# Kernel tuning notes

Measured on AMD Instinct MI355X. Metric: run time of the kernel, lower is better.

The kernel has to match this reference:

```python
import jax, jax.numpy as jnp
import numpy as np

B, N, D, P, H = 16, 1024, 512, 512, 8
E = P // H  # head dim = 64


def layer_norm(x, g, b, eps=1e-5):
    mu = jnp.mean(x, axis=-1, keepdims=True)
    var = jnp.var(x, axis=-1, keepdims=True)
    return (x - mu) * jax.lax.rsqrt(var + eps) * g + b


def setup_inputs() -> dict:
    key = jax.random.key(0)
    ks = jax.random.split(key, 12)
    s = 0.02
    inp = {
        "x": jax.random.normal(ks[0], (B, N, D), dtype=jnp.float32),
        "Wq": jax.random.normal(ks[1], (D, P), dtype=jnp.float32) * s,
        "bq": jnp.zeros((P,), jnp.float32),
        "Wk": jax.random.normal(ks[2], (D, P), dtype=jnp.float32) * s,
        "bk": jnp.zeros((P,), jnp.float32),
        "Wv": jax.random.normal(ks[3], (D, P), dtype=jnp.float32) * s,
        "bv": jnp.zeros((P,), jnp.float32),
        "Wo": jax.random.normal(ks[4], (P, D), dtype=jnp.float32) * s,
        "bo": jnp.zeros((D,), jnp.float32),
        "ln1_g": jnp.ones((D,), jnp.float32),
        "ln1_b": jnp.zeros((D,), jnp.float32),
        "W1": jax.random.normal(ks[5], (D, 4 * D), dtype=jnp.float32) * s,
        "b1": jnp.zeros((4 * D,), jnp.float32),
        "W2": jax.random.normal(ks[6], (4 * D, D), dtype=jnp.float32) * s,
        "b2": jnp.zeros((D,), jnp.float32),
        "ln2_g": jnp.ones((D,), jnp.float32),
        "ln2_b": jnp.zeros((D,), jnp.float32),
    }
    return inp


def reference(x, Wq, bq, Wk, bk, Wv, bv, Wo, bo, ln1_g, ln1_b, W1, b1, W2, b2, ln2_g, ln2_b):
    # dropout layers are identity in eval mode
    q = (x @ Wq + bq).reshape(B, N, H, E)
    k = (x @ Wk + bk).reshape(B, N, H, E)
    v = (x @ Wv + bv).reshape(B, N, H, E)
    scale = 1.0 / jnp.sqrt(jnp.float32(E))
    scores = jnp.einsum('blhe,bshe->bhls', q, k)  # [B,H,L,S]
    A = jax.nn.softmax(scale * scores, axis=-1)
    V = jnp.einsum('bhls,bshd->blhd', A, v).reshape(B, N, P)
    att = V @ Wo + bo
    x1 = layer_norm(x + att, ln1_g, ln1_b)
    # FFN: 1x1 convs over channel dim == per-token linears, exact GELU
    ff = jax.nn.gelu(x1 @ W1 + b1, approximate=False) @ W2 + b2
    return layer_norm(x1 + ff, ln2_g, ln2_b)
```

## Files before the change

kernel.cpp:

```cpp
#include <hip/hip_runtime.h>
#include <hip/hip_bf16.h>

typedef __hip_bfloat16 bf16;
typedef __bf16 bf16x8 __attribute__((ext_vector_type(8)));
typedef __bf16 bf16x4 __attribute__((ext_vector_type(4)));
typedef float f32x4 __attribute__((ext_vector_type(4)));

static __device__ __forceinline__ f32x4 mfma16(bf16x8 a, bf16x8 b, f32x4 c) {
  return __builtin_amdgcn_mfma_f32_16x16x32_bf16(a, b, c, 0, 0, 0);
}
static __device__ __forceinline__ bf16x8 ld8(const bf16* p) {
  return *reinterpret_cast<const bf16x8*>(p);
}
static __device__ __forceinline__ float toF(float v) { return v; }
static __device__ __forceinline__ float toF(bf16 v) { return __bfloat162float(v); }
static __device__ __forceinline__ void stF(float* p, float v) { *p = v; }
static __device__ __forceinline__ void stF(bf16* p, float v) { *p = __float2bfloat16(v); }

typedef __attribute__((address_space(1))) void gvoid;
typedef __attribute__((address_space(3))) void lvoid;
static __device__ __forceinline__ void gl2lds16(const bf16* g, bf16* l) {
  __builtin_amdgcn_global_load_lds((gvoid*)g, (lvoid*)l, 16, 0, 0);
}

__global__ __launch_bounds__(256) void cvt_kernel(const float* __restrict__ in,
                                                  bf16* __restrict__ out) {
  long i = (long)blockIdx.x * 256 + threadIdx.x;
  float4 v = reinterpret_cast<const float4*>(in)[i];
  bf16x4 o;
  o[0] = __float2bfloat16(v.x); o[1] = __float2bfloat16(v.y);
  o[2] = __float2bfloat16(v.z); o[3] = __float2bfloat16(v.w);
  reinterpret_cast<bf16x4*>(out)[i] = o;
}

__global__ void prep_weights(const float* __restrict__ Wq, const float* __restrict__ Wk,
                             const float* __restrict__ Wv, const float* __restrict__ Wo,
                             const float* __restrict__ W1, const float* __restrict__ W2,
                             bf16* __restrict__ Wtqkv, bf16* __restrict__ WtO,
                             bf16* __restrict__ Wt1, bf16* __restrict__ Wt2) {
  int id = blockIdx.x;
  const float* in;
  bf16* out;
  int K, N, n0, k0;
  if (id < 1024) {
    int which = id >> 8, t = id & 255;
    K = 512; N = 512;
    n0 = (t & 15) * 32; k0 = (t >> 4) * 32;
    if (which == 0)      { in = Wq; out = Wtqkv; }
    else if (which == 1) { in = Wk; out = Wtqkv + (size_t)512 * 512; }
    else if (which == 2) { in = Wv; out = Wtqkv + (size_t)1024 * 512; }
    else                 { in = Wo; out = WtO; }
  } else if (id < 2048) {
    int t = id - 1024;
    in = W1; out = Wt1; K = 512; N = 2048;
    n0 = (t & 63) * 32; k0 = (t >> 6) * 32;
  } else {
    int t = id - 2048;
    in = W2; out = Wt2; K = 2048; N = 512;
    n0 = (t & 15) * 32; k0 = (t >> 4) * 32;
  }
  __shared__ float tile[32][33];
  int tx = threadIdx.x, ty = threadIdx.y;
#pragma unroll
  for (int j = 0; j < 32; j += 8)
    tile[ty + j][tx] = in[(long)(k0 + ty + j) * N + n0 + tx];
  __syncthreads();
#pragma unroll
  for (int j = 0; j < 32; j += 8)
    out[(long)(n0 + ty + j) * K + k0 + tx] = __float2bfloat16(tile[tx][ty + j]);
}

template <int MODE>
__global__ __launch_bounds__(256) void gemm_kernel(
    const bf16* __restrict__ A, const bf16* __restrict__ Wt,
    const float* __restrict__ b0, const float* __restrict__ b1_,
    const float* __restrict__ b2_, bf16* C0, bf16* C1, bf16* C2,
    int K, int ldc, int mmask, int mshift) {
  __shared__ alignas(16) bf16 As[2][128 * 32];
  __shared__ alignas(16) bf16 Bs[2][128 * 32];
  const int tid = threadIdx.x;
  const int wave = tid >> 6, lane = tid & 63;
  const int lr = lane & 15, lq = lane >> 4;
  const int L = blockIdx.x;
  const int m0 = (L & mmask) * 128, n0 = (L >> mshift) * 128;
  const int wm = (wave >> 1) * 64, wn = (wave & 1) * 64;

  const int srow0 = (wave * 2) * 16 + (lane >> 2);
  const int srow1 = (wave * 2 + 1) * 16 + (lane >> 2);
  const int scol = (lane & 3) * 8;
  const bf16* Ag0 = A + (long)(m0 + srow0) * K + scol;
  const bf16* Ag1 = A + (long)(m0 + srow1) * K + scol;
  const bf16* Bg0 = Wt + (long)(n0 + srow0) * K + scol;
  const bf16* Bg1 = Wt + (long)(n0 + srow1) * K + scol;
  const int so0 = (wave * 2) * 16 * 32;
  const int so1 = (wave * 2 + 1) * 16 * 32;

  f32x4 acc[4][4] = {};

  gl2lds16(Ag0, &As[0][so0]);
  gl2lds16(Ag1, &As[0][so1]);
  gl2lds16(Bg0, &Bs[0][so0]);
  gl2lds16(Bg1, &Bs[0][so1]);
  __syncthreads();

  int p = 0;
  for (int k0 = 0; k0 < K; k0 += 32) {
    int kn = k0 + 32;
    if (kn < K) {
      gl2lds16(Ag0 + kn, &As[p ^ 1][so0]);
      gl2lds16(Ag1 + kn, &As[p ^ 1][so1]);
      gl2lds16(Bg0 + kn, &Bs[p ^ 1][so0]);
      gl2lds16(Bg1 + kn, &Bs[p ^ 1][so1]);
    }
    bf16x8 af[4], bfr[4];
#pragma unroll
    for (int i = 0; i < 4; ++i) af[i] = ld8(&As[p][(wm + i * 16 + lr) * 32 + lq * 8]);
#pragma unroll
    for (int j = 0; j < 4; ++j) bfr[j] = ld8(&Bs[p][(wn + j * 16 + lr) * 32 + lq * 8]);
#pragma unroll
    for (int i = 0; i < 4; ++i)
#pragma unroll
      for (int j = 0; j < 4; ++j) acc[i][j] = mfma16(af[i], bfr[j], acc[i][j]);
    __syncthreads();
    p ^= 1;
  }

  const float* bias = b0;
  bf16* C = C0;
  int cb = n0;
  bool vmode = false;
  if (MODE == 2) {
    if (n0 >= 1024)     { bias = b2_; C = C2; cb = n0 - 1024; vmode = true; }
    else if (n0 >= 512) { bias = b1_; C = C1; cb = n0 - 512; }
  }

#pragma unroll
  for (int i = 0; i < 4; ++i) {
#pragma unroll
    for (int j = 0; j < 4; ++j) {
      int col = cb + wn + j * 16 + lr;
      float bv = bias[col];
#pragma unroll
      for (int rr = 0; rr < 4; ++rr) {
        int row = m0 + wm + i * 16 + lq * 4 + rr;
        float v = acc[i][j][rr] + bv;
        if (MODE == 1) v = 0.5f * v * (1.0f + erff(v * 0.70710678118654752f));
        if (MODE == 2 && vmode) {
          int hh = col >> 6, e = col & 63;
          int bb = row >> 10, tok = row & 1023;
          C[(((long)((bb * 8 + hh) * 64 + e)) << 10) + tok] = __float2bfloat16(v);
        } else {
          C[(long)row * ldc + col] = __float2bfloat16(v);
        }
      }
    }
  }
}

__global__ __launch_bounds__(256) void attn_splitk(
    const bf16* __restrict__ Q, const bf16* __restrict__ Km,
    const bf16* __restrict__ Vt, bf16* __restrict__ Op,
    float* __restrict__ lsum) {
  constexpr int SP = 72;
  __shared__ alignas(16) bf16 Pall[4][64 * SP];
  const int tid = threadIdx.x;
  const int wave = tid >> 6, lane = tid & 63;
  const int lr = lane & 15, lq = lane >> 4;
  const int L = blockIdx.x;
  const int bh = ((L >> 6) << 3) | (L & 7);
  const int qh = (L >> 3) & 7;
  const int qc = qh & 3, half = qh >> 2;
  const int h = bh & 7, b = bh >> 3;
  const int q0 = qc * 256 + wave * 64;
  bf16* P = Pall[wave];
  const float Cc = 0.18033688011112042f;

  bf16x8 qf[4][2];
#pragma unroll
  for (int qs = 0; qs < 4; ++qs) {
    const bf16* qrow = Q + (long)(b * 1024 + q0 + qs * 16 + lr) * 512 + h * 64;
    qf[qs][0] = ld8(qrow + lq * 8);
    qf[qs][1] = ld8(qrow + 32 + lq * 8);
  }
  const bf16* kbase = Km + (long)(b * 1024 + half * 512) * 512 + h * 64;
  const bf16* vbase = Vt + (long)((b * 8 + h) * 64) * 1024 + half * 512;

  bf16x8 ones;
#pragma unroll
  for (int k = 0; k < 8; ++k) ones[k] = __float2bfloat16(1.0f);

  f32x4 oacc[4][4] = {};
  f32x4 lacc[4] = {};

  for (int kb = 0; kb < 8; ++kb) {
#pragma unroll
    for (int kt = 0; kt < 4; ++kt) {
      const bf16* krow = kbase + (long)(kb * 64 + kt * 16 + lr) * 512;
      bf16x8 kf0 = ld8(krow + lq * 8);
      bf16x8 kf1 = ld8(krow + 32 + lq * 8);
#pragma unroll
      for (int qs = 0; qs < 4; ++qs) {
        f32x4 t = {};
        t = mfma16(kf0, qf[qs][0], t);
        t = mfma16(kf1, qf[qs][1], t);
        bf16x4 pk;
#pragma unroll
        for (int rr = 0; rr < 4; ++rr) pk[rr] = __float2bfloat16(exp2f(t[rr] * Cc));
        *reinterpret_cast<bf16x4*>(&P[(qs * 16 + lr) * SP + kt * 16 + lq * 4]) = pk;
      }
    }
    __builtin_amdgcn_sched_barrier(0);
    bf16x8 pf[4][2];
#pragma unroll
    for (int qs = 0; qs < 4; ++qs) {
      pf[qs][0] = ld8(&P[(qs * 16 + lr) * SP + lq * 8]);
      pf[qs][1] = ld8(&P[(qs * 16 + lr) * SP + 32 + lq * 8]);
    }
#pragma unroll
    for (int qs = 0; qs < 4; ++qs) {
      lacc[qs] = mfma16(pf[qs][0], ones, lacc[qs]);
      lacc[qs] = mfma16(pf[qs][1], ones, lacc[qs]);
    }
#pragma unroll
    for (int j0 = 0; j0 < 4; ++j0) {
      const bf16* vrow = vbase + (long)(j0 * 16 + lr) * 1024 + kb * 64;
      bf16x8 vf0 = ld8(vrow + lq * 8);
      bf16x8 vf1 = ld8(vrow + 32 + lq * 8);
#pragma unroll
      for (int qs = 0; qs < 4; ++qs) {
        oacc[qs][j0] = mfma16(pf[qs][0], vf0, oacc[qs][j0]);
        oacc[qs][j0] = mfma16(pf[qs][1], vf1, oacc[qs][j0]);
      }
    }
    __builtin_amdgcn_sched_barrier(0);
  }

  bf16* Oh = Op + (size_t)half * ((size_t)16384 * 512);
#pragma unroll
  for (int qs = 0; qs < 4; ++qs)
#pragma unroll
    for (int rr = 0; rr < 4; ++rr)
#pragma unroll
      for (int j0 = 0; j0 < 4; ++j0)
        Oh[(long)(b * 1024 + q0 + qs * 16 + lq * 4 + rr) * 512 + h * 64 + j0 * 16 + lr] =
            __float2bfloat16(oacc[qs][j0][rr]);
  if (lr == 0) {
    float* lp = lsum + (size_t)half * 131072 + ((size_t)(b * 8 + h) << 10);
#pragma unroll
    for (int qs = 0; qs < 4; ++qs)
#pragma unroll
      for (int rr = 0; rr < 4; ++rr)
        lp[q0 + qs * 16 + lq * 4 + rr] = lacc[qs][rr];
  }
}

__global__ __launch_bounds__(256) void attn_combine(
    const bf16* __restrict__ Op, const float* __restrict__ lsum,
    bf16* __restrict__ O) {
  long i = (long)blockIdx.x * 256 + threadIdx.x;
  long idx = i * 8;
  int tok = (int)(idx >> 9), col = (int)(idx & 511);
  int b = tok >> 10, q = tok & 1023, h = col >> 6;
  int li = (b * 8 + h) * 1024 + q;
  float inv = 1.0f / (lsum[li] + lsum[131072 + li]);
  bf16x8 a = ld8(Op + idx);
  bf16x8 c = ld8(Op + (size_t)16384 * 512 + idx);
  bf16x8 o;
#pragma unroll
  for (int k = 0; k < 8; ++k)
    o[k] = __float2bfloat16(((float)a[k] + (float)c[k]) * inv);
  *reinterpret_cast<bf16x8*>(O + idx) = o;
}

__global__ __launch_bounds__(256) void attn_kernel(
    const bf16* Q, const bf16* __restrict__ Km,
    const bf16* __restrict__ Vt, bf16* O) {
  constexpr int SP = 72;
  __shared__ alignas(16) bf16 Pall[4][64 * SP];
  const int tid = threadIdx.x;
  const int wave = tid >> 6, lane = tid & 63;
  const int lr = lane & 15, lq = lane >> 4;
  const int L = blockIdx.x;
  const int bh = ((L >> 5) << 3) | (L & 7);
  const int qc = (L >> 3) & 3;
  const int h = bh & 7, b = bh >> 3;
  const int q0 = qc * 256 + wave * 64;
  bf16* P = Pall[wave];
  const float Cc = 0.18033688011112042f;

  bf16x8 qf[4][2];
#pragma unroll
  for (int qs = 0; qs < 4; ++qs) {
    const bf16* qrow = Q + (long)(b * 1024 + q0 + qs * 16 + lr) * 512 + h * 64;
    qf[qs][0] = ld8(qrow + lq * 8);
    qf[qs][1] = ld8(qrow + 32 + lq * 8);
  }
  const bf16* kbase = Km + (long)(b * 1024) * 512 + h * 64;
  const bf16* vbase = Vt + (long)((b * 8 + h) * 64) * 1024;

  bf16x8 ones;
#pragma unroll
  for (int k = 0; k < 8; ++k) ones[k] = __float2bfloat16(1.0f);

  f32x4 oacc[4][4] = {};
  f32x4 lacc[4] = {};

  for (int kb = 0; kb < 16; ++kb) {
#pragma unroll
    for (int kt = 0; kt < 4; ++kt) {
      const bf16* krow = kbase + (long)(kb * 64 + kt * 16 + lr) * 512;
      bf16x8 kf0 = ld8(krow + lq * 8);
      bf16x8 kf1 = ld8(krow + 32 + lq * 8);
#pragma unroll
      for (int qs = 0; qs < 4; ++qs) {
        f32x4 t = {};
        t = mfma16(kf0, qf[qs][0], t);
        t = mfma16(kf1, qf[qs][1], t);
        bf16x4 pk;
#pragma unroll
        for (int rr = 0; rr < 4; ++rr) pk[rr] = __float2bfloat16(exp2f(t[rr] * Cc));
        *reinterpret_cast<bf16x4*>(&P[(qs * 16 + lr) * SP + kt * 16 + lq * 4]) = pk;
      }
    }
    __builtin_amdgcn_sched_barrier(0);
    bf16x8 pf[4][2];
#pragma unroll
    for (int qs = 0; qs < 4; ++qs) {
      pf[qs][0] = ld8(&P[(qs * 16 + lr) * SP + lq * 8]);
      pf[qs][1] = ld8(&P[(qs * 16 + lr) * SP + 32 + lq * 8]);
    }
#pragma unroll
    for (int qs = 0; qs < 4; ++qs) {
      lacc[qs] = mfma16(pf[qs][0], ones, lacc[qs]);
      lacc[qs] = mfma16(pf[qs][1], ones, lacc[qs]);
    }
#pragma unroll
    for (int j0 = 0; j0 < 4; ++j0) {
      const bf16* vrow = vbase + (long)(j0 * 16 + lr) * 1024 + kb * 64;
      bf16x8 vf0 = ld8(vrow + lq * 8);
      bf16x8 vf1 = ld8(vrow + 32 + lq * 8);
#pragma unroll
      for (int qs = 0; qs < 4; ++qs) {
        oacc[qs][j0] = mfma16(pf[qs][0], vf0, oacc[qs][j0]);
        oacc[qs][j0] = mfma16(pf[qs][1], vf1, oacc[qs][j0]);
      }
    }
    __builtin_amdgcn_sched_barrier(0);
  }

#pragma unroll
  for (int qs = 0; qs < 4; ++qs)
#pragma unroll
    for (int rr = 0; rr < 4; ++rr) {
      float lv = 1.0f / lacc[qs][rr];
#pragma unroll
      for (int j0 = 0; j0 < 4; ++j0)
        O[(long)(b * 1024 + q0 + qs * 16 + lq * 4 + rr) * 512 + h * 64 + j0 * 16 + lr] =
            __float2bfloat16(oacc[qs][j0][rr] * lv);
    }
}

template <typename TX, typename TO>
__global__ __launch_bounds__(256) void add_ln_kernel(
    const TX* __restrict__ X, const bf16* __restrict__ Y,
    const float* __restrict__ g, const float* __restrict__ bb,
    TO* __restrict__ out) {
  const int row = blockIdx.x, t = threadIdx.x;
  __shared__ float s1[4], s2[4];
  long base = (long)row * 512;
  float v0 = toF(X[base + t]) + toF(Y[base + t]);
  float v1 = toF(X[base + 256 + t]) + toF(Y[base + 256 + t]);
  float s = v0 + v1, q = v0 * v0 + v1 * v1;
#pragma unroll
  for (int o = 32; o > 0; o >>= 1) {
    s += __shfl_down(s, o);
    q += __shfl_down(q, o);
  }
  int wv = t >> 6;
  if ((t & 63) == 0) { s1[wv] = s; s2[wv] = q; }
  __syncthreads();
  float St = s1[0] + s1[1] + s1[2] + s1[3];
  float Qt = s2[0] + s2[1] + s2[2] + s2[3];
  float mean = St * (1.f / 512.f);
  float var = Qt * (1.f / 512.f) - mean * mean;
  float rs = rsqrtf(var + 1e-5f);
  stF(&out[base + t], (v0 - mean) * rs * g[t] + bb[t]);
  stF(&out[base + 256 + t], (v1 - mean) * rs * g[256 + t] + bb[256 + t]);
}

extern "C" void kernel_launch(void* const* d_in, const int* in_sizes, int n_in,
                              void* d_out, int out_size, void* d_ws, size_t ws_size,
                              hipStream_t stream) {
  const float* x    = (const float*)d_in[0];
  const float* Wq   = (const float*)d_in[1];
  const float* bq   = (const float*)d_in[2];
  const float* Wk   = (const float*)d_in[3];
  const float* bk   = (const float*)d_in[4];
  const float* Wv   = (const float*)d_in[5];
  const float* bv   = (const float*)d_in[6];
  const float* Wo   = (const float*)d_in[7];
  const float* bo   = (const float*)d_in[8];
  const float* ln1g = (const float*)d_in[9];
  const float* ln1b = (const float*)d_in[10];
  const float* W1   = (const float*)d_in[11];
  const float* b1   = (const float*)d_in[12];
  const float* W2   = (const float*)d_in[13];
  const float* b2   = (const float*)d_in[14];
  const float* ln2g = (const float*)d_in[15];
  const float* ln2b = (const float*)d_in[16];
  float* out = (float*)d_out;

  char* ws = (char*)d_ws;
  size_t off = 0;
  auto alloc = [&](size_t bytes) {
    char* p = ws + off;
    off += (bytes + 255) & ~(size_t)255;
    return (bf16*)p;
  };
  bf16* Wtqkv = alloc((size_t)1536 * 512 * 2);
  bf16* WtO   = alloc((size_t)512 * 512 * 2);
  bf16* Wt1   = alloc((size_t)512 * 2048 * 2);
  bf16* Wt2   = alloc((size_t)2048 * 512 * 2);
  const size_t SB = (size_t)16384 * 512 * 2;

  dim3 tb(32, 8);

  if (ws_size >= (size_t)104 * 1024 * 1024) {
    bf16* xb  = alloc(SB);
    bf16* kb  = alloc(SB);
    bf16* qb  = alloc(SB);
    bf16* vtb = alloc(SB);
    bf16* p0  = alloc(SB);
    bf16* p1  = alloc(SB);
    float* lsum = (float*)alloc((size_t)2 * 131072 * 4);
    bf16* ff1 = qb;
    bf16* ff2 = xb;
    (void)p1;

    cvt_kernel<<<8192, 256, 0, stream>>>(x, xb);
    prep_weights<<<3072, tb, 0, stream>>>(Wq, Wk, Wv, Wo, W1, W2,
                                          Wtqkv, WtO, Wt1, Wt2);
    gemm_kernel<2><<<1536, 256, 0, stream>>>(xb, Wtqkv, bq, bk, bv,
                                             qb, kb, vtb, 512, 512, 127, 7);
    attn_splitk<<<1024, 256, 0, stream>>>(qb, kb, vtb, p0, lsum);
    attn_combine<<<4096, 256, 0, stream>>>(p0, lsum, qb);
    gemm_kernel<0><<<512, 256, 0, stream>>>(qb, WtO, bo, nullptr, nullptr,
                                            vtb, nullptr, nullptr, 512, 512, 127, 7);
    add_ln_kernel<bf16, bf16><<<16384, 256, 0, stream>>>(xb, vtb, ln1g, ln1b, kb);
    gemm_kernel<1><<<2048, 256, 0, stream>>>(kb, Wt1, b1, nullptr, nullptr,
                                             ff1, nullptr, nullptr, 512, 2048, 127, 7);
    gemm_kernel<0><<<512, 256, 0, stream>>>(ff1, Wt2, b2, nullptr, nullptr,
                                            ff2, nullptr, nullptr, 2048, 512, 127, 7);
    add_ln_kernel<bf16, float><<<16384, 256, 0, stream>>>(kb, ff2, ln2g, ln2b, out);
  } else {
    bf16* xb  = alloc(SB);
    bf16* kb  = alloc(SB);
    bf16* qb  = alloc(SB);
    bf16* vtb = alloc(SB);
    bf16* fb  = alloc(SB / 2);
    bf16* ff1 = qb;

    cvt_kernel<<<8192, 256, 0, stream>>>(x, xb);
    prep_weights<<<3072, tb, 0, stream>>>(Wq, Wk, Wv, Wo, W1, W2,
                                          Wtqkv, WtO, Wt1, Wt2);
    gemm_kernel<2><<<1536, 256, 0, stream>>>(xb, Wtqkv, bq, bk, bv,
                                             qb, kb, vtb, 512, 512, 127, 7);
    attn_kernel<<<512, 256, 0, stream>>>(qb, kb, vtb, qb);
    gemm_kernel<0><<<512, 256, 0, stream>>>(qb, WtO, bo, nullptr, nullptr,
                                            vtb, nullptr, nullptr, 512, 512, 127, 7);
    add_ln_kernel<bf16, bf16><<<16384, 256, 0, stream>>>(xb, vtb, ln1g, ln1b, kb);

    for (int hh = 0; hh < 2; ++hh) {
      const bf16* x1h = kb + (size_t)hh * 8192 * 512;
      gemm_kernel<1><<<1024, 256, 0, stream>>>(x1h, Wt1, b1, nullptr, nullptr,
                                               ff1, nullptr, nullptr, 512, 2048, 63, 6);
      gemm_kernel<0><<<256, 256, 0, stream>>>(ff1, Wt2, b2, nullptr, nullptr,
                                              fb, nullptr, nullptr, 2048, 512, 63, 6);
      add_ln_kernel<bf16, float><<<8192, 256, 0, stream>>>(x1h, fb, ln2g, ln2b,
                                                           out + (size_t)hh * 8192 * 512);
    }
  }
}
```

Before: 409.1 us.

## Rewrite attention with 32x32 MFMA, register-only P via permlane swap, no split-K

Replaces the split-K attention and its combine kernel with one kernel that gives each wave 32 queries over the full key range, using 32x32x16 MFMA. The probability tile is repacked in registers with permlane32_swap instead of going through LDS, and the row sum is accumulated on scalar ALUs rather than with an extra MFMA against a ones vector. This removes the partial-output round trip to memory, the combine launch and the LDS traffic. In exchange each wave holds a smaller query tile, so K/V reuse per load drops, and the dependency chain inside each wave is longer.

```diff
diff --git a/kernel.cpp b/kernel.cpp
--- a/kernel.cpp
+++ b/kernel.cpp
@@ -5,9 +5,14 @@
 typedef __bf16 bf16x8 __attribute__((ext_vector_type(8)));
 typedef __bf16 bf16x4 __attribute__((ext_vector_type(4)));
 typedef float f32x4 __attribute__((ext_vector_type(4)));
+typedef float f32x16 __attribute__((ext_vector_type(16)));
+typedef unsigned u32x4 __attribute__((ext_vector_type(4)));
 
 static __device__ __forceinline__ f32x4 mfma16(bf16x8 a, bf16x8 b, f32x4 c) {
   return __builtin_amdgcn_mfma_f32_16x16x32_bf16(a, b, c, 0, 0, 0);
+}
+static __device__ __forceinline__ f32x16 mfma32(bf16x8 a, bf16x8 b, f32x16 c) {
+  return __builtin_amdgcn_mfma_f32_32x32x16_bf16(a, b, c, 0, 0, 0);
 }
 static __device__ __forceinline__ bf16x8 ld8(const bf16* p) {
   return *reinterpret_cast<const bf16x8*>(p);
@@ -16,6 +21,11 @@
 static __device__ __forceinline__ float toF(bf16 v) { return __bfloat162float(v); }
 static __device__ __forceinline__ void stF(float* p, float v) { *p = v; }
 static __device__ __forceinline__ void stF(bf16* p, float v) { *p = __float2bfloat16(v); }
+static __device__ __forceinline__ unsigned pk2(float lo, float hi) {
+  unsigned a = __bfloat16_as_ushort(__float2bfloat16(lo));
+  unsigned b = __bfloat16_as_ushort(__float2bfloat16(hi));
+  return (b << 16) | a;
+}
 
 typedef __attribute__((address_space(1))) void gvoid;
 typedef __attribute__((address_space(3))) void lvoid;
@@ -157,207 +167,94 @@
   }
 }
 
-__global__ __launch_bounds__(256) void attn_splitk(
+__global__ __launch_bounds__(256, 4) void attn32(
     const bf16* __restrict__ Q, const bf16* __restrict__ Km,
-    const bf16* __restrict__ Vt, bf16* __restrict__ Op,
-    float* __restrict__ lsum) {
-  constexpr int SP = 72;
-  __shared__ alignas(16) bf16 Pall[4][64 * SP];
+    const bf16* __restrict__ Vt, bf16* __restrict__ O) {
+  __shared__ alignas(16) float lred[4][32];
   const int tid = threadIdx.x;
   const int wave = tid >> 6, lane = tid & 63;
-  const int lr = lane & 15, lq = lane >> 4;
-  const int L = blockIdx.x;
-  const int bh = ((L >> 6) << 3) | (L & 7);
-  const int qh = (L >> 3) & 7;
-  const int qc = qh & 3, half = qh >> 2;
+  const int l31 = lane & 31, lh = lane >> 5;
+  const int bi = blockIdx.x;
+  const int bh = bi & 127;
+  const int qt = (bi >> 7) * 4 + wave;
   const int h = bh & 7, b = bh >> 3;
-  const int q0 = qc * 256 + wave * 64;
-  bf16* P = Pall[wave];
+  const int q0 = qt * 32;
   const float Cc = 0.18033688011112042f;
 
-  bf16x8 qf[4][2];
-#pragma unroll
-  for (int qs = 0; qs < 4; ++qs) {
-    const bf16* qrow = Q + (long)(b * 1024 + q0 + qs * 16 + lr) * 512 + h * 64;
-    qf[qs][0] = ld8(qrow + lq * 8);
-    qf[qs][1] = ld8(qrow + 32 + lq * 8);
-  }
-  const bf16* kbase = Km + (long)(b * 1024 + half * 512) * 512 + h * 64;
-  const bf16* vbase = Vt + (long)((b * 8 + h) * 64) * 1024 + half * 512;
-
-  bf16x8 ones;
-#pragma unroll
-  for (int k = 0; k < 8; ++k) ones[k] = __float2bfloat16(1.0f);
-
-  f32x4 oacc[4][4] = {};
-  f32x4 lacc[4] = {};
-
-  for (int kb = 0; kb < 8; ++kb) {
-#pragma unroll
-    for (int kt = 0; kt < 4; ++kt) {
-      const bf16* krow = kbase + (long)(kb * 64 + kt * 16 + lr) * 512;
-      bf16x8 kf0 = ld8(krow + lq * 8);
-      bf16x8 kf1 = ld8(krow + 32 + lq * 8);
-#pragma unroll
-      for (int qs = 0; qs < 4; ++qs) {
-        f32x4 t = {};
-        t = mfma16(kf0, qf[qs][0], t);
-        t = mfma16(kf1, qf[qs][1], t);
-        bf16x4 pk;
-#pragma unroll
-        for (int rr = 0; rr < 4; ++rr) pk[rr] = __float2bfloat16(exp2f(t[rr] * Cc));
-        *reinterpret_cast<bf16x4*>(&P[(qs * 16 + lr) * SP + kt * 16 + lq * 4]) = pk;
-      }
+  bf16x8 qf[4];
+  const bf16* qp = Q + (long)(b * 1024 + q0 + l31) * 512 + h * 64 + lh * 8;
+#pragma unroll
+  for (int et = 0; et < 4; ++et) qf[et] = ld8(qp + et * 16);
+
+  const bf16* kpt = Km + (long)(b * 1024 + l31) * 512 + h * 64 + lh * 8;
+  const bf16* vp0 = Vt + ((long)((b * 8 + h) * 64 + l31)) * 1024 + lh * 8;
+  const bf16* vp1 = vp0 + (long)32 * 1024;
+
+  f32x16 oacc[2] = {};
+  float lsum = 0.f;
+
+  for (int t = 0; t < 32; ++t) {
+    bf16x8 kf[4], vf0a, vf0b, vf1a, vf1b;
+#pragma unroll
+    for (int et = 0; et < 4; ++et) kf[et] = ld8(kpt + et * 16);
+    vf0a = ld8(vp0);
+    vf0b = ld8(vp0 + 16);
+    vf1a = ld8(vp1);
+    vf1b = ld8(vp1 + 16);
+
+    f32x16 s = {};
+#pragma unroll
+    for (int et = 0; et < 4; ++et) s = mfma32(kf[et], qf[et], s);
+
+    float pr[16];
+#pragma unroll
+    for (int r = 0; r < 16; ++r) { pr[r] = exp2f(s[r] * Cc); lsum += pr[r]; }
+
+    unsigned w0 = pk2(pr[0], pr[1]),   w1 = pk2(pr[2], pr[3]);
+    unsigned w2 = pk2(pr[4], pr[5]),   w3 = pk2(pr[6], pr[7]);
+    unsigned w4 = pk2(pr[8], pr[9]),   w5 = pk2(pr[10], pr[11]);
+    unsigned w6 = pk2(pr[12], pr[13]), w7 = pk2(pr[14], pr[15]);
+    auto r02 = __builtin_amdgcn_permlane32_swap(w0, w2, false, false);
+    auto r13 = __builtin_amdgcn_permlane32_swap(w1, w3, false, false);
+    auto r46 = __builtin_amdgcn_permlane32_swap(w4, w6, false, false);
+    auto r57 = __builtin_amdgcn_permlane32_swap(w5, w7, false, false);
+    u32x4 a0 = {r02[0], r13[0], r02[1], r13[1]};
+    u32x4 a1 = {r46[0], r57[0], r46[1], r57[1]};
+    bf16x8 pf0 = __builtin_bit_cast(bf16x8, a0);
+    bf16x8 pf1 = __builtin_bit_cast(bf16x8, a1);
+
+    oacc[0] = mfma32(pf0, vf0a, oacc[0]);
+    oacc[1] = mfma32(pf0, vf1a, oacc[1]);
+    oacc[0] = mfma32(pf1, vf0b, oacc[0]);
+    oacc[1] = mfma32(pf1, vf1b, oacc[1]);
+
+    kpt += 32 * 512;
+    vp0 += 32;
+    vp1 += 32;
+  }
+
+  lsum += __shfl_xor(lsum, 32);
+  if (lh == 0) lred[wave][l31] = lsum;
+  __syncthreads();
+
+  float linv[16];
+#pragma unroll
+  for (int g = 0; g < 4; ++g) {
+    f32x4 lvv = *(const f32x4*)&lred[wave][g * 8 + 4 * lh];
+#pragma unroll
+    for (int j = 0; j < 4; ++j) linv[g * 4 + j] = 1.f / lvv[j];
+  }
+
+  const long rowbase = (long)(b * 1024 + q0);
+#pragma unroll
+  for (int et = 0; et < 2; ++et) {
+    bf16* obase = O + rowbase * 512 + h * 64 + et * 32 + l31;
+#pragma unroll
+    for (int r = 0; r < 16; ++r) {
+      int q = (r & 3) + 8 * (r >> 2) + 4 * lh;
+      obase[(long)q * 512] = __float2bfloat16(oacc[et][r] * linv[r]);
     }
-    __builtin_amdgcn_sched_barrier(0);
-    bf16x8 pf[4][2];
-#pragma unroll
-    for (int qs = 0; qs < 4; ++qs) {
-      pf[qs][0] = ld8(&P[(qs * 16 + lr) * SP + lq * 8]);
-      pf[qs][1] = ld8(&P[(qs * 16 + lr) * SP + 32 + lq * 8]);
-    }
-#pragma unroll
-    for (int qs = 0; qs < 4; ++qs) {
-      lacc[qs] = mfma16(pf[qs][0], ones, lacc[qs]);
-      lacc[qs] = mfma16(pf[qs][1], ones, lacc[qs]);
-    }
-#pragma unroll
-    for (int j0 = 0; j0 < 4; ++j0) {
-      const bf16* vrow = vbase + (long)(j0 * 16 + lr) * 1024 + kb * 64;
-      bf16x8 vf0 = ld8(vrow + lq * 8);
-      bf16x8 vf1 = ld8(vrow + 32 + lq * 8);
-#pragma unroll
-      for (int qs = 0; qs < 4; ++qs) {
-        oacc[qs][j0] = mfma16(pf[qs][0], vf0, oacc[qs][j0]);
-        oacc[qs][j0] = mfma16(pf[qs][1], vf1, oacc[qs][j0]);
-      }
-    }
-    __builtin_amdgcn_sched_barrier(0);
-  }
-
-  bf16* Oh = Op + (size_t)half * ((size_t)16384 * 512);
-#pragma unroll
-  for (int qs = 0; qs < 4; ++qs)
-#pragma unroll
-    for (int rr = 0; rr < 4; ++rr)
-#pragma unroll
-      for (int j0 = 0; j0 < 4; ++j0)
-        Oh[(long)(b * 1024 + q0 + qs * 16 + lq * 4 + rr) * 512 + h * 64 + j0 * 16 + lr] =
-            __float2bfloat16(oacc[qs][j0][rr]);
-  if (lr == 0) {
-    float* lp = lsum + (size_t)half * 131072 + ((size_t)(b * 8 + h) << 10);
-#pragma unroll
-    for (int qs = 0; qs < 4; ++qs)
-#pragma unroll
-      for (int rr = 0; rr < 4; ++rr)
-        lp[q0 + qs * 16 + lq * 4 + rr] = lacc[qs][rr];
-  }
-}
-
-__global__ __launch_bounds__(256) void attn_combine(
-    const bf16* __restrict__ Op, const float* __restrict__ lsum,
-    bf16* __restrict__ O) {
-  long i = (long)blockIdx.x * 256 + threadIdx.x;
-  long idx = i * 8;
-  int tok = (int)(idx >> 9), col = (int)(idx & 511);
-  int b = tok >> 10, q = tok & 1023, h = col >> 6;
-  int li = (b * 8 + h) * 1024 + q;
-  float inv = 1.0f / (lsum[li] + lsum[131072 + li]);
-  bf16x8 a = ld8(Op + idx);
-  bf16x8 c = ld8(Op + (size_t)16384 * 512 + idx);
-  bf16x8 o;
-#pragma unroll
-  for (int k = 0; k < 8; ++k)
-    o[k] = __float2bfloat16(((float)a[k] + (float)c[k]) * inv);
-  *reinterpret_cast<bf16x8*>(O + idx) = o;
-}
-
-__global__ __launch_bounds__(256) void attn_kernel(
-    const bf16* Q, const bf16* __restrict__ Km,
-    const bf16* __restrict__ Vt, bf16* O) {
-  constexpr int SP = 72;
-  __shared__ alignas(16) bf16 Pall[4][64 * SP];
-  const int tid = threadIdx.x;
-  const int wave = tid >> 6, lane = tid & 63;
-  const int lr = lane & 15, lq = lane >> 4;
-  const int L = blockIdx.x;
-  const int bh = ((L >> 5) << 3) | (L & 7);
-  const int qc = (L >> 3) & 3;
-  const int h = bh & 7, b = bh >> 3;
-  const int q0 = qc * 256 + wave * 64;
-  bf16* P = Pall[wave];
-  const float Cc = 0.18033688011112042f;
-
-  bf16x8 qf[4][2];
-#pragma unroll
-  for (int qs = 0; qs < 4; ++qs) {
-    const bf16* qrow = Q + (long)(b * 1024 + q0 + qs * 16 + lr) * 512 + h * 64;
-    qf[qs][0] = ld8(qrow + lq * 8);
-    qf[qs][1] = ld8(qrow + 32 + lq * 8);
-  }
-  const bf16* kbase = Km + (long)(b * 1024) * 512 + h * 64;
-  const bf16* vbase = Vt + (long)((b * 8 + h) * 64) * 1024;
-
-  bf16x8 ones;
-#pragma unroll
-  for (int k = 0; k < 8; ++k) ones[k] = __float2bfloat16(1.0f);
-
-  f32x4 oacc[4][4] = {};
-  f32x4 lacc[4] = {};
-
-  for (int kb = 0; kb < 16; ++kb) {
-#pragma unroll
-    for (int kt = 0; kt < 4; ++kt) {
-      const bf16* krow = kbase + (long)(kb * 64 + kt * 16 + lr) * 512;
-      bf16x8 kf0 = ld8(krow + lq * 8);
-      bf16x8 kf1 = ld8(krow + 32 + lq * 8);
-#pragma unroll
-      for (int qs = 0; qs < 4; ++qs) {
-        f32x4 t = {};
-        t = mfma16(kf0, qf[qs][0], t);
-        t = mfma16(kf1, qf[qs][1], t);
-        bf16x4 pk;
-#pragma unroll
-        for (int rr = 0; rr < 4; ++rr) pk[rr] = __float2bfloat16(exp2f(t[rr] * Cc));
-        *reinterpret_cast<bf16x4*>(&P[(qs * 16 + lr) * SP + kt * 16 + lq * 4]) = pk;
-      }
-    }
-    __builtin_amdgcn_sched_barrier(0);
-    bf16x8 pf[4][2];
-#pragma unroll
-    for (int qs = 0; qs < 4; ++qs) {
-      pf[qs][0] = ld8(&P[(qs * 16 + lr) * SP + lq * 8]);
-      pf[qs][1] = ld8(&P[(qs * 16 + lr) * SP + 32 + lq * 8]);
-    }
-#pragma unroll
-    for (int qs = 0; qs < 4; ++qs) {
-      lacc[qs] = mfma16(pf[qs][0], ones, lacc[qs]);
-      lacc[qs] = mfma16(pf[qs][1], ones, lacc[qs]);
-    }
-#pragma unroll
-    for (int j0 = 0; j0 < 4; ++j0) {
-      const bf16* vrow = vbase + (long)(j0 * 16 + lr) * 1024 + kb * 64;
-      bf16x8 vf0 = ld8(vrow + lq * 8);
-      bf16x8 vf1 = ld8(vrow + 32 + lq * 8);
-#pragma unroll
-      for (int qs = 0; qs < 4; ++qs) {
-        oacc[qs][j0] = mfma16(pf[qs][0], vf0, oacc[qs][j0]);
-        oacc[qs][j0] = mfma16(pf[qs][1], vf1, oacc[qs][j0]);
-      }
-    }
-    __builtin_amdgcn_sched_barrier(0);
-  }
-
-#pragma unroll
-  for (int qs = 0; qs < 4; ++qs)
-#pragma unroll
-    for (int rr = 0; rr < 4; ++rr) {
-      float lv = 1.0f / lacc[qs][rr];
-#pragma unroll
-      for (int j0 = 0; j0 < 4; ++j0)
-        O[(long)(b * 1024 + q0 + qs * 16 + lq * 4 + rr) * 512 + h * 64 + j0 * 16 + lr] =
-            __float2bfloat16(oacc[qs][j0][rr] * lv);
-    }
+  }
 }
 
 template <typename TX, typename TO>
@@ -432,18 +329,16 @@
     bf16* vtb = alloc(SB);
     bf16* p0  = alloc(SB);
     bf16* p1  = alloc(SB);
-    float* lsum = (float*)alloc((size_t)2 * 131072 * 4);
     bf16* ff1 = qb;
     bf16* ff2 = xb;
-    (void)p1;
+    (void)p0; (void)p1;
 
     cvt_kernel<<<8192, 256, 0, stream>>>(x, xb);
     prep_weights<<<3072, tb, 0, stream>>>(Wq, Wk, Wv, Wo, W1, W2,
                                           Wtqkv, WtO, Wt1, Wt2);
     gemm_kernel<2><<<1536, 256, 0, stream>>>(xb, Wtqkv, bq, bk, bv,
                                              qb, kb, vtb, 512, 512, 127, 7);
-    attn_splitk<<<1024, 256, 0, stream>>>(qb, kb, vtb, p0, lsum);
-    attn_combine<<<4096, 256, 0, stream>>>(p0, lsum, qb);
+    attn32<<<1024, 256, 0, stream>>>(qb, kb, vtb, qb);
     gemm_kernel<0><<<512, 256, 0, stream>>>(qb, WtO, bo, nullptr, nullptr,
                                             vtb, nullptr, nullptr, 512, 512, 127, 7);
     add_ln_kernel<bf16, bf16><<<16384, 256, 0, stream>>>(xb, vtb, ln1g, ln1b, kb);
@@ -465,7 +360,7 @@
                                           Wtqkv, WtO, Wt1, Wt2);
     gemm_kernel<2><<<1536, 256, 0, stream>>>(xb, Wtqkv, bq, bk, bv,
                                              qb, kb, vtb, 512, 512, 127, 7);
-    attn_kernel<<<512, 256, 0, stream>>>(qb, kb, vtb, qb);
+    attn32<<<1024, 256, 0, stream>>>(qb, kb, vtb, qb);
     gemm_kernel<0><<<512, 256, 0, stream>>>(qb, WtO, bo, nullptr, nullptr,
                                             vtb, nullptr, nullptr, 512, 512, 127, 7);
     add_ln_kernel<bf16, bf16><<<16384, 256, 0, stream>>>(xb, vtb, ln1g, ln1b, kb);
```

Result: slower. 438.5 us (+7.2%).

## Stage K/V tiles into LDS with double-buffered async loads in attention

Applied to the files above, without the earlier changes.

The attention kernel now loads each 64-row K and V tile cooperatively into shared memory using global_load_lds, double-buffered so the next tile is prefetched while the current one is used. Before this, each of the four waves loaded the same K/V data directly from global memory, so the block fetched it four times. The change removes that redundant traffic and overlaps loads with compute. In exchange it adds a block-wide barrier every iteration and uses more LDS, which could lower occupancy.

```diff
diff --git a/kernel.cpp b/kernel.cpp
--- a/kernel.cpp
+++ b/kernel.cpp
@@ -163,6 +163,8 @@
     float* __restrict__ lsum) {
   constexpr int SP = 72;
   __shared__ alignas(16) bf16 Pall[4][64 * SP];
+  __shared__ alignas(16) bf16 Ks[2][2][64][32];
+  __shared__ alignas(16) bf16 Vs[2][2][64][32];
   const int tid = threadIdx.x;
   const int wave = tid >> 6, lane = tid & 63;
   const int lr = lane & 15, lq = lane >> 4;
@@ -185,6 +187,20 @@
   const bf16* kbase = Km + (long)(b * 1024 + half * 512) * 512 + h * 64;
   const bf16* vbase = Vt + (long)((b * 8 + h) * 64) * 1024 + half * 512;
 
+  const int sr = wave * 16 + (lane >> 2);
+  const int sc = (lane & 3) * 8;
+  const bf16* Kg = kbase + (long)sr * 512 + sc;
+  const bf16* Vg = vbase + (long)sr * 1024 + sc;
+
+  auto stage = [&](int kb, int p) {
+#pragma unroll
+    for (int kk = 0; kk < 2; ++kk)
+      gl2lds16(Kg + (long)kb * 64 * 512 + kk * 32, &Ks[p][kk][wave * 16][0]);
+#pragma unroll
+    for (int kk = 0; kk < 2; ++kk)
+      gl2lds16(Vg + kb * 64 + kk * 32, &Vs[p][kk][wave * 16][0]);
+  };
+
   bf16x8 ones;
 #pragma unroll
   for (int k = 0; k < 8; ++k) ones[k] = __float2bfloat16(1.0f);
@@ -192,12 +208,16 @@
   f32x4 oacc[4][4] = {};
   f32x4 lacc[4] = {};
 
+  stage(0, 0);
+  __syncthreads();
+
+  int p = 0;
   for (int kb = 0; kb < 8; ++kb) {
+    if (kb < 7) stage(kb + 1, p ^ 1);
 #pragma unroll
     for (int kt = 0; kt < 4; ++kt) {
-      const bf16* krow = kbase + (long)(kb * 64 + kt * 16 + lr) * 512;
-      bf16x8 kf0 = ld8(krow + lq * 8);
-      bf16x8 kf1 = ld8(krow + 32 + lq * 8);
+      bf16x8 kf0 = ld8(&Ks[p][0][kt * 16 + lr][lq * 8]);
+      bf16x8 kf1 = ld8(&Ks[p][1][kt * 16 + lr][lq * 8]);
 #pragma unroll
       for (int qs = 0; qs < 4; ++qs) {
         f32x4 t = {};
@@ -223,9 +243,8 @@
     }
 #pragma unroll
     for (int j0 = 0; j0 < 4; ++j0) {
-      const bf16* vrow = vbase + (long)(j0 * 16 + lr) * 1024 + kb * 64;
-      bf16x8 vf0 = ld8(vrow + lq * 8);
-      bf16x8 vf1 = ld8(vrow + 32 + lq * 8);
+      bf16x8 vf0 = ld8(&Vs[p][0][j0 * 16 + lr][lq * 8]);
+      bf16x8 vf1 = ld8(&Vs[p][1][j0 * 16 + lr][lq * 8]);
 #pragma unroll
       for (int qs = 0; qs < 4; ++qs) {
         oacc[qs][j0] = mfma16(pf[qs][0], vf0, oacc[qs][j0]);
@@ -233,6 +252,8 @@
       }
     }
     __builtin_amdgcn_sched_barrier(0);
+    __syncthreads();
+    p ^= 1;
   }
 
   bf16* Oh = Op + (size_t)half * ((size_t)16384 * 512);
```

After: 401.4 us. No clear change (-1.9%).
